# Kernel optimization log

Measured on AMD Instinct MI355X. Metric: run time of the kernel, lower is better.

Reference implementation:

```python
import jax, jax.numpy as jnp
import numpy as np

SELF_DIM = 64
NB_DIM = 64
HID = 256
K = 16  # num_use_neighbor_obs


def _ff(x, w1, b1, w2, b2):
    # FeedForward: Linear -> GELU (exact erf, torch nn.GELU default) -> Linear
    return jax.nn.gelu(x @ w1 + b1, approximate=False) @ w2 + b2


def setup_inputs() -> dict:
    key = jax.random.key(0)
    ks = jax.random.split(key, 9)
    B = 8192
    s = 0.02
    return {
        "self_obs": jax.random.normal(ks[0], (B, SELF_DIM), jnp.float32),
        "obs": jax.random.normal(ks[1], (B, SELF_DIM + K * NB_DIM), jnp.float32),
        "We1": jax.random.normal(ks[2], (SELF_DIM + NB_DIM, 4 * (SELF_DIM + NB_DIM)), jnp.float32) * s,
        "be1": jnp.zeros((4 * (SELF_DIM + NB_DIM),), jnp.float32),
        "We2": jax.random.normal(ks[3], (4 * (SELF_DIM + NB_DIM), HID), jnp.float32) * s,
        "be2": jnp.zeros((HID,), jnp.float32),
        "Wv1": jax.random.normal(ks[4], (HID, 4 * HID), jnp.float32) * s,
        "bv1": jnp.zeros((4 * HID,), jnp.float32),
        "Wv2": jax.random.normal(ks[5], (4 * HID, HID), jnp.float32) * s,
        "bv2": jnp.zeros((HID,), jnp.float32),
        "Wa1": jax.random.normal(ks[6], (2 * HID, 8 * HID), jnp.float32) * s,
        "ba1": jnp.zeros((8 * HID,), jnp.float32),
        "Wa2": jax.random.normal(ks[7], (8 * HID, 1), jnp.float32) * s,
        "ba2": jnp.zeros((1,), jnp.float32),
        "all_neighbor_obs_size": K * NB_DIM,
        "batch_size": 8192,
    }


def reference(self_obs, obs, We1, be1, We2, be2, Wv1, bv1, Wv2, bv2,
              Wa1, ba1, Wa2, ba2, all_neighbor_obs_size, batch_size):
    # neighbor obs: (B, K*nd) -> (B*K, nd), batch-major row order
    obs_neighbors = obs[:, SELF_DIM:SELF_DIM + all_neighbor_obs_size].reshape(-1, NB_DIM)
    # torch .repeat(K, 1): tiles the whole batch K times -> neighbor-major order
    self_obs_repeat = jnp.tile(self_obs, (K, 1))  # (K*B, self_dim)
    mlp_input = jnp.concatenate([self_obs_repeat, obs_neighbors], axis=1)
    neighbor_embeddings = _ff(mlp_input, We1, be1, We2, be2)          # (B*K, H)
    neighbor_values = _ff(neighbor_embeddings, Wv1, bv1, Wv2, bv2)    # (B*K, H)
    emb_mean = neighbor_embeddings.reshape(batch_size, -1, HID).mean(axis=1)  # (B, H)
    emb_mean_repeat = jnp.tile(emb_mean, (K, 1))                      # (K*B, H)
    attn_in = jnp.concatenate([neighbor_embeddings, emb_mean_repeat], axis=1)
    attn_logits = _ff(attn_in, Wa1, ba1, Wa2, ba2).reshape(batch_size, -1)  # (B, K)
    attn = jax.nn.softmax(attn_logits, axis=1).reshape(-1, 1)         # (B*K, 1)
    final = (attn * neighbor_values).reshape(batch_size, -1, HID).sum(axis=1)
    return final
```

## Files before the change

### kernel.cpp

```cpp
#include <hip/hip_runtime.h>
#include <hip/hip_bf16.h>

#define B_SZ 8192
#define KNB 16
#define BK 131072
#define ED 256

typedef __attribute__((ext_vector_type(8))) short short8v;
typedef __attribute__((ext_vector_type(4))) float floatx4;

static __device__ __forceinline__ unsigned short f2bf(float f) {
  unsigned int u = __float_as_uint(f);
  u = (u + 0x7FFFu + ((u >> 16) & 1u)) >> 16;
  return (unsigned short)u;
}
static __device__ __forceinline__ float bf2f(unsigned short u) {
  return __uint_as_float(((unsigned int)u) << 16);
}
static __device__ __forceinline__ float gelu_erf(float x) {
  return 0.5f * x * (1.0f + erff(x * 0.70710678118654752f));
}
static __device__ __forceinline__ float gelu_poly(float x) {
  float t = x * x;
  float p = fmaf(t, fmaf(t, fmaf(t, fmaf(t, 2.8935185185e-4f, -2.9761904762e-3f),
                                 2.5e-2f), -1.6666666667e-1f), 1.0f);
  return 0.5f * x * fmaf(0.79788456080286536f * x, p, 1.0f);
}

#define MFMA(a, b, c) __builtin_amdgcn_mfma_f32_16x16x32_bf16((a), (b), (c), 0, 0, 0)

static __device__ __forceinline__ void gll16(const void* g, void* l) {
  __builtin_amdgcn_global_load_lds(
      (const __attribute__((address_space(1))) unsigned int*)g,
      (__attribute__((address_space(3))) unsigned int*)l, 16, 0, 0);
}

__global__ void wt_kernel(const float* __restrict__ W, unsigned short* __restrict__ WT,
                          int K, int N) {
  int idx = blockIdx.x * 256 + threadIdx.x;
  if (idx >= K * N) return;
  int n = idx / K, k = idx - n * K;
  WT[idx] = f2bf(W[(size_t)k * N + n]);
}

__global__ __launch_bounds__(256) void k1_kernel(
    const float* __restrict__ self_obs, const float* __restrict__ obs,
    const unsigned short* __restrict__ We1T, const float* __restrict__ be1,
    const unsigned short* __restrict__ We2T, const float* __restrict__ be2,
    unsigned short* __restrict__ E, unsigned short* __restrict__ M) {
  __shared__ unsigned short Xt[64][136];
  __shared__ unsigned short Ht[64][136];
  const int tid = threadIdx.x;
  const int wave = tid >> 6, lane = tid & 63, g = lane >> 4, r = lane & 15;
  const int row0 = blockIdx.x * 64;

#pragma unroll
  for (int p = 0; p < 8; ++p) {
    int e4 = (p * 256 + tid) * 4;
    int i = e4 >> 7, c = e4 & 127;
    int gi = row0 + i;
    const float* src;
    if (c < 64) src = self_obs + (size_t)(gi & (B_SZ - 1)) * 64 + c;
    else        src = obs + (size_t)(gi >> 4) * 1088 + 64 + (gi & 15) * 64 + (c - 64);
    float4 v = *(const float4*)src;
    ushort4 w;
    w.x = f2bf(v.x); w.y = f2bf(v.y); w.z = f2bf(v.z); w.w = f2bf(v.w);
    *(ushort4*)&Xt[i][c] = w;
  }
  __syncthreads();

  floatx4 eacc[4][4];
#pragma unroll
  for (int a = 0; a < 4; ++a)
#pragma unroll
    for (int c2 = 0; c2 < 4; ++c2) eacc[a][c2] = (floatx4)0.0f;

  for (int chunk = 0; chunk < 4; ++chunk) {
    const int hbase = chunk * 128;
    floatx4 hacc[2][4];
#pragma unroll
    for (int a = 0; a < 2; ++a)
#pragma unroll
      for (int c2 = 0; c2 < 4; ++c2) hacc[a][c2] = (floatx4)0.0f;

#pragma unroll
    for (int kk = 0; kk < 4; ++kk) {
      short8v afr[4];
#pragma unroll
      for (int rt = 0; rt < 4; ++rt)
        afr[rt] = *(const short8v*)&Xt[rt * 16 + r][kk * 32 + g * 8];
#pragma unroll
      for (int ctl = 0; ctl < 2; ++ctl) {
        int col = hbase + wave * 32 + ctl * 16 + r;
        short8v bfr = *(const short8v*)&We1T[(size_t)col * 128 + kk * 32 + g * 8];
#pragma unroll
        for (int rt = 0; rt < 4; ++rt) hacc[ctl][rt] = MFMA(afr[rt], bfr, hacc[ctl][rt]);
      }
    }
#pragma unroll
    for (int ctl = 0; ctl < 2; ++ctl) {
      int col = hbase + wave * 32 + ctl * 16 + r;
      float bias = be1[col];
#pragma unroll
      for (int rt = 0; rt < 4; ++rt)
#pragma unroll
        for (int q = 0; q < 4; ++q) {
          float h = gelu_erf(hacc[ctl][rt][q] + bias);
          Ht[rt * 16 + g * 4 + q][wave * 32 + ctl * 16 + r] = f2bf(h);
        }
    }
    __syncthreads();
#pragma unroll
    for (int kk = 0; kk < 4; ++kk) {
      short8v afr[4];
#pragma unroll
      for (int rt = 0; rt < 4; ++rt)
        afr[rt] = *(const short8v*)&Ht[rt * 16 + r][kk * 32 + g * 8];
#pragma unroll
      for (int ct = 0; ct < 4; ++ct) {
        int col = wave * 64 + ct * 16 + r;
        short8v bfr = *(const short8v*)&We2T[(size_t)col * 512 + hbase + kk * 32 + g * 8];
#pragma unroll
        for (int rt = 0; rt < 4; ++rt) eacc[rt][ct] = MFMA(afr[rt], bfr, eacc[rt][ct]);
      }
    }
    __syncthreads();
  }

#pragma unroll
  for (int ct = 0; ct < 4; ++ct) {
    int col = wave * 64 + ct * 16 + r;
    float bias = be2[col];
#pragma unroll
    for (int rt = 0; rt < 4; ++rt) {
      float msum = 0.f;
#pragma unroll
      for (int q = 0; q < 4; ++q) {
        float e = eacc[rt][ct][q] + bias;
        int row = rt * 16 + g * 4 + q;
        E[(size_t)(row0 + row) * ED + col] = f2bf(e);
        msum += e;
      }
      msum += __shfl_xor(msum, 16);
      msum += __shfl_xor(msum, 32);
      if (g == 0) {
        int b = (row0 >> 4) + rt;
        M[(size_t)b * ED + col] = f2bf(msum * 0.0625f);
      }
    }
  }
}

__global__ __launch_bounds__(512) void k2_mv(
    const unsigned short* __restrict__ M, const unsigned short* __restrict__ Wa1T,
    const float* __restrict__ ba1, unsigned short* __restrict__ MV) {
  __shared__ unsigned short Abuf[128 * 64];
  __shared__ unsigned short Bbuf[256 * 64];
  const int tid = threadIdx.x;
  const int wave = tid >> 6, lane = tid & 63, g = lane >> 4, r = lane & 15;
  const int wr = wave >> 2, wc = wave & 3;
  const int row0 = blockIdx.y * 128;
  const int col0 = blockIdx.x * 256;
  const int sr = lane >> 3, sc = lane & 7;
  const int swz = ((sc ^ sr) << 4);

  floatx4 acc[4][4];
#pragma unroll
  for (int a = 0; a < 4; ++a)
#pragma unroll
    for (int c2 = 0; c2 < 4; ++c2) acc[a][c2] = (floatx4)0.0f;

  for (int t = 0; t < 4; ++t) {
#pragma unroll
    for (int j = 0; j < 2; ++j) {
      int rowA = j * 64 + wave * 8 + sr;
      const char* src = (const char*)M + ((size_t)(row0 + rowA)) * 512 + t * 128 + swz;
      gll16(src, (char*)Abuf + (j * 512 + wave * 64) * 16);
    }
#pragma unroll
    for (int j = 0; j < 4; ++j) {
      int colB = j * 64 + wave * 8 + sr;
      const char* src = (const char*)Wa1T + ((size_t)(col0 + colB)) * 1024 + 512
                        + t * 128 + swz;
      gll16(src, (char*)Bbuf + (j * 512 + wave * 64) * 16);
    }
    __syncthreads();
#pragma unroll
    for (int kk = 0; kk < 2; ++kk) {
      const int off = (kk * 64 + g * 16) ^ ((r & 7) << 4);
      short8v afr[4], bfr[4];
#pragma unroll
      for (int rt = 0; rt < 4; ++rt)
        afr[rt] = *(const short8v*)((const char*)Abuf + (wr * 64 + rt * 16 + r) * 128 + off);
#pragma unroll
      for (int ct = 0; ct < 4; ++ct)
        bfr[ct] = *(const short8v*)((const char*)Bbuf + (wc * 64 + ct * 16 + r) * 128 + off);
#pragma unroll
      for (int rt = 0; rt < 4; ++rt)
#pragma unroll
        for (int ct = 0; ct < 4; ++ct) acc[rt][ct] = MFMA(afr[rt], bfr[ct], acc[rt][ct]);
    }
    __syncthreads();
  }

#pragma unroll
  for (int ct = 0; ct < 4; ++ct) {
    int col = col0 + wc * 64 + ct * 16 + r;
    float b1 = ba1[col];
#pragma unroll
    for (int rt = 0; rt < 4; ++rt)
#pragma unroll
      for (int q = 0; q < 4; ++q)
        MV[(size_t)(row0 + wr * 64 + rt * 16 + g * 4 + q) * 2048 + col] =
            f2bf(acc[rt][ct][q] + b1);
  }
}

__global__ __launch_bounds__(512, 4) void k3_fused(
    const unsigned short* __restrict__ E, const unsigned short* __restrict__ MV,
    const unsigned short* __restrict__ Wa1T, const float* __restrict__ Wa2,
    float* __restrict__ L) {
  __shared__ char Bq[65536];
  const int tid = threadIdx.x;
  const int wave = tid >> 6, lane = tid & 63, g = lane >> 4, r = lane & 15;
  const int j = blockIdx.x * 8 + wave;
  const int xsw = (r & 7) << 4;

  const unsigned short* ebase = E + ((size_t)r * 8192 + j) * 256 + g * 8;
  short8v er[8];
#pragma unroll
  for (int kk = 0; kk < 8; ++kk) er[kk] = *(const short8v*)(ebase + kk * 32);

  const int scol2 = lane >> 5;
  const int sbyte = (lane & 31) * 16;

  auto STAGE = [&](int c, int bufsel) {
#pragma unroll
    for (int cc = 0; cc < 4; ++cc) {
      int m = wave * 4 + cc;
      int col = c * 64 + m * 2 + scol2;
      const char* src = (const char*)Wa1T + (size_t)col * 1024
                        + (sbyte ^ ((col & 7) << 4));
      gll16(src, Bq + bufsel * 32768 + m * 1024);
    }
  };

  STAGE(0, 0);
  __syncthreads();

  float lg = 0.f;
  const unsigned short* mvrow = MV + (size_t)j * 2048;

  for (int c = 0; c < 32; ++c) {
    if (c + 1 < 32) STAGE(c + 1, (c + 1) & 1);
    ushort4 mvu[4];
    float4 w2[4];
#pragma unroll
    for (int ct = 0; ct < 4; ++ct) {
      mvu[ct] = *(const ushort4*)(mvrow + c * 64 + ct * 16 + g * 4);
      w2[ct] = *(const float4*)&Wa2[c * 64 + ct * 16 + g * 4];
    }
    floatx4 acc[4];
#pragma unroll
    for (int ct = 0; ct < 4; ++ct) acc[ct] = (floatx4)0.0f;
    const char* bufb = Bq + (c & 1) * 32768;
#pragma unroll
    for (int kk = 0; kk < 8; ++kk) {
      const int off = (kk * 64 + g * 16) ^ xsw;
#pragma unroll
      for (int ct = 0; ct < 4; ++ct) {
        short8v a = *(const short8v*)(bufb + (ct * 16 + r) * 512 + off);
        acc[ct] = MFMA(a, er[kk], acc[ct]);
      }
    }
#pragma unroll
    for (int ct = 0; ct < 4; ++ct) {
      const float* wp = (const float*)&w2[ct];
      lg = fmaf(gelu_poly(acc[ct][0] + bf2f(mvu[ct].x)), wp[0], lg);
      lg = fmaf(gelu_poly(acc[ct][1] + bf2f(mvu[ct].y)), wp[1], lg);
      lg = fmaf(gelu_poly(acc[ct][2] + bf2f(mvu[ct].z)), wp[2], lg);
      lg = fmaf(gelu_poly(acc[ct][3] + bf2f(mvu[ct].w)), wp[3], lg);
    }
    __syncthreads();
  }

  lg += __shfl_xor(lg, 16);
  lg += __shfl_xor(lg, 32);
  if (g == 0) L[(size_t)r * 8192 + j] = lg;
}

__global__ __launch_bounds__(256) void k4_softmax(
    const float* __restrict__ L, const float* __restrict__ ba2,
    float* __restrict__ attnw) {
  int row = blockIdx.x * 256 + threadIdx.x;
  float logit = L[row] + ba2[0];
  float m = logit;
  m = fmaxf(m, __shfl_xor(m, 1)); m = fmaxf(m, __shfl_xor(m, 2));
  m = fmaxf(m, __shfl_xor(m, 4)); m = fmaxf(m, __shfl_xor(m, 8));
  float e = expf(logit - m);
  float s = e;
  s += __shfl_xor(s, 1); s += __shfl_xor(s, 2);
  s += __shfl_xor(s, 4); s += __shfl_xor(s, 8);
  attnw[row] = e / s;
}

__global__ __launch_bounds__(512) void k5a_gemm(
    const unsigned short* __restrict__ E, const unsigned short* __restrict__ Wv1T,
    const float* __restrict__ bv1, const float* __restrict__ attnw,
    unsigned short* __restrict__ G) {
  __shared__ unsigned short Abuf[128 * 64];
  __shared__ unsigned short Bbuf[256 * 64];
  const int tid = threadIdx.x;
  const int wave = tid >> 6, lane = tid & 63, g = lane >> 4, r = lane & 15;
  const int wr = wave >> 2, wc = wave & 3;
  const int nb = blockIdx.x;
  const int row0 = blockIdx.y * 128;
  const int col0 = nb * 256;
  const int sr = lane >> 3, sc = lane & 7;
  const int swz = ((sc ^ sr) << 4);

  floatx4 acc[4][4];
#pragma unroll
  for (int a = 0; a < 4; ++a)
#pragma unroll
    for (int c2 = 0; c2 < 4; ++c2) acc[a][c2] = (floatx4)0.0f;

  for (int t = 0; t < 4; ++t) {
#pragma unroll
    for (int j = 0; j < 2; ++j) {
      int rowA = j * 64 + wave * 8 + sr;
      const char* src = (const char*)E + ((size_t)(row0 + rowA)) * 512 + t * 128 + swz;
      gll16(src, (char*)Abuf + (j * 512 + wave * 64) * 16);
    }
#pragma unroll
    for (int j = 0; j < 4; ++j) {
      int colB = j * 64 + wave * 8 + sr;
      const char* src = (const char*)Wv1T + ((size_t)(col0 + colB)) * 512 + t * 128 + swz;
      gll16(src, (char*)Bbuf + (j * 512 + wave * 64) * 16);
    }
    __syncthreads();
#pragma unroll
    for (int kk = 0; kk < 2; ++kk) {
      const int off = (kk * 64 + g * 16) ^ ((r & 7) << 4);
      short8v afr[4], bfr[4];
#pragma unroll
      for (int rt = 0; rt < 4; ++rt)
        afr[rt] = *(const short8v*)((const char*)Abuf + (wr * 64 + rt * 16 + r) * 128 + off);
#pragma unroll
      for (int ct = 0; ct < 4; ++ct)
        bfr[ct] = *(const short8v*)((const char*)Bbuf + (wc * 64 + ct * 16 + r) * 128 + off);
#pragma unroll
      for (int rt = 0; rt < 4; ++rt)
#pragma unroll
        for (int ct = 0; ct < 4; ++ct) acc[rt][ct] = MFMA(afr[rt], bfr[ct], acc[rt][ct]);
    }
    __syncthreads();
  }

  float aw[4][4];
#pragma unroll
  for (int rt = 0; rt < 4; ++rt)
#pragma unroll
    for (int q = 0; q < 4; ++q)
      aw[rt][q] = attnw[row0 + wr * 64 + rt * 16 + g * 4 + q];
#pragma unroll
  for (int ct = 0; ct < 4; ++ct) {
    int col = col0 + wc * 64 + ct * 16 + r;
    float b1 = bv1[col];
#pragma unroll
    for (int rt = 0; rt < 4; ++rt) {
      float s = 0.f;
#pragma unroll
      for (int q = 0; q < 4; ++q)
        s = fmaf(aw[rt][q], gelu_poly(acc[rt][ct][q] + b1), s);
      s += __shfl_xor(s, 16);
      s += __shfl_xor(s, 32);
      if (g == 0)
        G[(size_t)((row0 >> 4) + wr * 4 + rt) * 1024 + col] = f2bf(s);
    }
  }
}

__global__ __launch_bounds__(256) void k5b_gemm(
    const unsigned short* __restrict__ G, const unsigned short* __restrict__ Wv2T,
    const float* __restrict__ bv2, float* __restrict__ out) {
  __shared__ unsigned short Abuf[64 * 64];
  __shared__ unsigned short Bbuf[128 * 64];
  const int tid = threadIdx.x;
  const int wave = tid >> 6, lane = tid & 63, g = lane >> 4, r = lane & 15;
  const int wr = wave >> 1, wc = wave & 1;
  const int col0 = blockIdx.x * 128;
  const int row0 = blockIdx.y * 64;
  const int sr = lane >> 3, sc = lane & 7;
  const int swz = ((sc ^ sr) << 4);

  floatx4 acc[2][4];
#pragma unroll
  for (int a = 0; a < 2; ++a)
#pragma unroll
    for (int c2 = 0; c2 < 4; ++c2) acc[a][c2] = (floatx4)0.0f;

  for (int t = 0; t < 16; ++t) {
#pragma unroll
    for (int j = 0; j < 2; ++j) {
      int rowA = j * 32 + wave * 8 + sr;
      const char* src = (const char*)G + ((size_t)(row0 + rowA)) * 2048 + t * 128 + swz;
      gll16(src, (char*)Abuf + (j * 256 + wave * 64) * 16);
    }
#pragma unroll
    for (int j = 0; j < 4; ++j) {
      int colB = j * 32 + wave * 8 + sr;
      const char* src = (const char*)Wv2T + ((size_t)(col0 + colB)) * 2048 + t * 128 + swz;
      gll16(src, (char*)Bbuf + (j * 256 + wave * 64) * 16);
    }
    __syncthreads();
#pragma unroll
    for (int kk = 0; kk < 2; ++kk) {
      const int off = (kk * 64 + g * 16) ^ ((r & 7) << 4);
      short8v afr[2], bfr[4];
#pragma unroll
      for (int rt = 0; rt < 2; ++rt)
        afr[rt] = *(const short8v*)((const char*)Abuf + (wr * 32 + rt * 16 + r) * 128 + off);
#pragma unroll
      for (int ct = 0; ct < 4; ++ct)
        bfr[ct] = *(const short8v*)((const char*)Bbuf + (wc * 64 + ct * 16 + r) * 128 + off);
#pragma unroll
      for (int rt = 0; rt < 2; ++rt)
#pragma unroll
        for (int ct = 0; ct < 4; ++ct) acc[rt][ct] = MFMA(afr[rt], bfr[ct], acc[rt][ct]);
    }
    __syncthreads();
  }

#pragma unroll
  for (int ct = 0; ct < 4; ++ct) {
    int col = col0 + wc * 64 + ct * 16 + r;
    float b = bv2[col];
#pragma unroll
    for (int rt = 0; rt < 2; ++rt)
#pragma unroll
      for (int q = 0; q < 4; ++q)
        out[(size_t)(row0 + wr * 32 + rt * 16 + g * 4 + q) * ED + col] =
            acc[rt][ct][q] + b;
  }
}

extern "C" void kernel_launch(void* const* d_in, const int* in_sizes, int n_in,
                              void* d_out, int out_size, void* d_ws, size_t ws_size,
                              hipStream_t stream) {
  const float* self_obs = (const float*)d_in[0];
  const float* obs = (const float*)d_in[1];
  const float* We1 = (const float*)d_in[2];
  const float* be1 = (const float*)d_in[3];
  const float* We2 = (const float*)d_in[4];
  const float* be2 = (const float*)d_in[5];
  const float* Wv1 = (const float*)d_in[6];
  const float* bv1 = (const float*)d_in[7];
  const float* Wv2 = (const float*)d_in[8];
  const float* bv2 = (const float*)d_in[9];
  const float* Wa1 = (const float*)d_in[10];
  const float* ba1 = (const float*)d_in[11];
  const float* Wa2 = (const float*)d_in[12];
  const float* ba2 = (const float*)d_in[13];
  float* out = (float*)d_out;

  char* ws = (char*)d_ws;
  size_t off = 0;
  auto alloc = [&](size_t bytes) {
    char* p = ws + off;
    off += (bytes + 255) & ~(size_t)255;
    return p;
  };
  unsigned short* E    = (unsigned short*)alloc((size_t)BK * ED * 2);
  unsigned short* M    = (unsigned short*)alloc((size_t)B_SZ * ED * 2);
  float*          attn = (float*)alloc((size_t)BK * 4);
  unsigned short* MV   = (unsigned short*)alloc((size_t)B_SZ * 2048 * 2);
  float*          L    = (float*)alloc((size_t)BK * 4);
  unsigned short* We1T = (unsigned short*)alloc(128 * 512 * 2);
  unsigned short* We2T = (unsigned short*)alloc(512 * 256 * 2);
  unsigned short* Wv1T = (unsigned short*)alloc(256 * 1024 * 2);
  unsigned short* Wv2T = (unsigned short*)alloc(1024 * 256 * 2);
  unsigned short* Wa1T = (unsigned short*)alloc(512 * 2048 * 2);
  unsigned short* G    = (unsigned short*)MV;

  wt_kernel<<<(128 * 512 + 255) / 256, 256, 0, stream>>>(We1, We1T, 128, 512);
  wt_kernel<<<(512 * 256 + 255) / 256, 256, 0, stream>>>(We2, We2T, 512, 256);
  wt_kernel<<<(256 * 1024 + 255) / 256, 256, 0, stream>>>(Wv1, Wv1T, 256, 1024);
  wt_kernel<<<(1024 * 256 + 255) / 256, 256, 0, stream>>>(Wv2, Wv2T, 1024, 256);
  wt_kernel<<<(512 * 2048 + 255) / 256, 256, 0, stream>>>(Wa1, Wa1T, 512, 2048);

  k1_kernel<<<BK / 64, 256, 0, stream>>>(self_obs, obs, We1T, be1, We2T, be2, E, M);
  k2_mv<<<dim3(8, 64), 512, 0, stream>>>(M, Wa1T, ba1, MV);
  k3_fused<<<B_SZ / 8, 512, 0, stream>>>(E, MV, Wa1T, Wa2, L);
  k4_softmax<<<BK / 256, 256, 0, stream>>>(L, ba2, attn);
  k5a_gemm<<<dim3(4, 1024), 512, 0, stream>>>(E, Wv1T, bv1, attn, G);
  k5b_gemm<<<dim3(2, 128), 256, 0, stream>>>(G, Wv2T, bv2, out);
}
```

Baseline: 504.2 us.

## Pre-swizzle Wa1 into MFMA fragment layout and process two batch rows per wave

A new prep kernel writes the first half of Wa1 (its first 256 input rows) into bf16 laid out in MFMA A-fragment order, so LDS staging and fragment reads become contiguous per-lane 16-byte accesses with no XOR swizzle. In k3 each wave now handles two batch columns, reusing every LDS-loaded weight fragment for two MFMAs. The column chunk shrinks from 64 to 32, which halves LDS use but doubles the number of loop iterations and barriers. Register pressure rises from holding two E fragment sets and two accumulator sets per wave, and the grid is halved.

```diff
diff --git a/kernel.cpp b/kernel.cpp
--- a/kernel.cpp
+++ b/kernel.cpp
@@ -41,6 +41,18 @@
   if (idx >= K * N) return;
   int n = idx / K, k = idx - n * K;
   WT[idx] = f2bf(W[(size_t)k * N + n]);
+}
+
+__global__ void wa1f_kernel(const float* __restrict__ Wa1,
+                            unsigned short* __restrict__ Wa1F) {
+  int idx = blockIdx.x * 256 + threadIdx.x;
+  int f = idx >> 9;
+  int w = idx & 511;
+  int ln = w >> 3, i = w & 7;
+  int ctile = f >> 3, kk = f & 7;
+  int col = ctile * 16 + (ln & 15);
+  int k = kk * 32 + (ln >> 4) * 8 + i;
+  Wa1F[idx] = f2bf(Wa1[(size_t)k * 2048 + col]);
 }
 
 __global__ __launch_bounds__(256) void k1_kernel(
@@ -218,75 +230,83 @@
 
 __global__ __launch_bounds__(512, 4) void k3_fused(
     const unsigned short* __restrict__ E, const unsigned short* __restrict__ MV,
-    const unsigned short* __restrict__ Wa1T, const float* __restrict__ Wa2,
+    const unsigned short* __restrict__ Wa1F, const float* __restrict__ Wa2,
     float* __restrict__ L) {
-  __shared__ char Bq[65536];
+  __shared__ char Bq[32768];
   const int tid = threadIdx.x;
   const int wave = tid >> 6, lane = tid & 63, g = lane >> 4, r = lane & 15;
-  const int j = blockIdx.x * 8 + wave;
-  const int xsw = (r & 7) << 4;
-
-  const unsigned short* ebase = E + ((size_t)r * 8192 + j) * 256 + g * 8;
-  short8v er[8];
-#pragma unroll
-  for (int kk = 0; kk < 8; ++kk) er[kk] = *(const short8v*)(ebase + kk * 32);
-
-  const int scol2 = lane >> 5;
-  const int sbyte = (lane & 31) * 16;
+  const int j0 = blockIdx.x * 16 + wave * 2;
+
+  short8v er0[8], er1[8];
+  {
+    const unsigned short* e0 = E + ((size_t)r * 8192 + j0) * 256 + g * 8;
+    const unsigned short* e1 = e0 + 256;
+#pragma unroll
+    for (int kk = 0; kk < 8; ++kk) {
+      er0[kk] = *(const short8v*)(e0 + kk * 32);
+      er1[kk] = *(const short8v*)(e1 + kk * 32);
+    }
+  }
 
   auto STAGE = [&](int c, int bufsel) {
 #pragma unroll
-    for (int cc = 0; cc < 4; ++cc) {
-      int m = wave * 4 + cc;
-      int col = c * 64 + m * 2 + scol2;
-      const char* src = (const char*)Wa1T + (size_t)col * 1024
-                        + (sbyte ^ ((col & 7) << 4));
-      gll16(src, Bq + bufsel * 32768 + m * 1024);
+    for (int cc = 0; cc < 2; ++cc) {
+      const char* src = (const char*)Wa1F + (size_t)c * 16384
+                        + (wave * 2 + cc) * 1024 + lane * 16;
+      gll16(src, Bq + bufsel * 16384 + (wave * 2 + cc) * 1024);
     }
   };
 
   STAGE(0, 0);
   __syncthreads();
 
-  float lg = 0.f;
-  const unsigned short* mvrow = MV + (size_t)j * 2048;
-
-  for (int c = 0; c < 32; ++c) {
-    if (c + 1 < 32) STAGE(c + 1, (c + 1) & 1);
-    ushort4 mvu[4];
-    float4 w2[4];
-#pragma unroll
-    for (int ct = 0; ct < 4; ++ct) {
-      mvu[ct] = *(const ushort4*)(mvrow + c * 64 + ct * 16 + g * 4);
-      w2[ct] = *(const float4*)&Wa2[c * 64 + ct * 16 + g * 4];
-    }
-    floatx4 acc[4];
-#pragma unroll
-    for (int ct = 0; ct < 4; ++ct) acc[ct] = (floatx4)0.0f;
-    const char* bufb = Bq + (c & 1) * 32768;
+  float lgp0 = 0.f, lgp1 = 0.f;
+  const unsigned short* mv0 = MV + (size_t)j0 * 2048;
+  const unsigned short* mv1 = mv0 + 2048;
+
+  for (int c = 0; c < 64; ++c) {
+    if (c + 1 < 64) STAGE(c + 1, (c + 1) & 1);
+    ushort4 mq0[2], mq1[2];
+    float4 w2[2];
+#pragma unroll
+    for (int ct = 0; ct < 2; ++ct) {
+      mq0[ct] = *(const ushort4*)(mv0 + c * 32 + ct * 16 + g * 4);
+      mq1[ct] = *(const ushort4*)(mv1 + c * 32 + ct * 16 + g * 4);
+      w2[ct] = *(const float4*)&Wa2[c * 32 + ct * 16 + g * 4];
+    }
+    floatx4 acc0[2], acc1[2];
+    acc0[0] = (floatx4)0.0f; acc0[1] = (floatx4)0.0f;
+    acc1[0] = (floatx4)0.0f; acc1[1] = (floatx4)0.0f;
+    const char* bufb = Bq + (c & 1) * 16384;
 #pragma unroll
     for (int kk = 0; kk < 8; ++kk) {
-      const int off = (kk * 64 + g * 16) ^ xsw;
-#pragma unroll
-      for (int ct = 0; ct < 4; ++ct) {
-        short8v a = *(const short8v*)(bufb + (ct * 16 + r) * 512 + off);
-        acc[ct] = MFMA(a, er[kk], acc[ct]);
+#pragma unroll
+      for (int ct = 0; ct < 2; ++ct) {
+        short8v a = *(const short8v*)(bufb + (ct * 8 + kk) * 1024 + lane * 16);
+        acc0[ct] = MFMA(a, er0[kk], acc0[ct]);
+        acc1[ct] = MFMA(a, er1[kk], acc1[ct]);
       }
     }
 #pragma unroll
-    for (int ct = 0; ct < 4; ++ct) {
+    for (int ct = 0; ct < 2; ++ct) {
       const float* wp = (const float*)&w2[ct];
-      lg = fmaf(gelu_poly(acc[ct][0] + bf2f(mvu[ct].x)), wp[0], lg);
-      lg = fmaf(gelu_poly(acc[ct][1] + bf2f(mvu[ct].y)), wp[1], lg);
-      lg = fmaf(gelu_poly(acc[ct][2] + bf2f(mvu[ct].z)), wp[2], lg);
-      lg = fmaf(gelu_poly(acc[ct][3] + bf2f(mvu[ct].w)), wp[3], lg);
-    }
-    __syncthreads();
-  }
-
-  lg += __shfl_xor(lg, 16);
-  lg += __shfl_xor(lg, 32);
-  if (g == 0) L[(size_t)r * 8192 + j] = lg;
+      const unsigned short* m0p = (const unsigned short*)&mq0[ct];
+      const unsigned short* m1p = (const unsigned short*)&mq1[ct];
+#pragma unroll
+      for (int q = 0; q < 4; ++q) {
+        lgp0 = fmaf(gelu_poly(acc0[ct][q] + bf2f(m0p[q])), wp[q], lgp0);
+        lgp1 = fmaf(gelu_poly(acc1[ct][q] + bf2f(m1p[q])), wp[q], lgp1);
+      }
+    }
+    __syncthreads();
+  }
+
+  lgp0 += __shfl_xor(lgp0, 16); lgp0 += __shfl_xor(lgp0, 32);
+  lgp1 += __shfl_xor(lgp1, 16); lgp1 += __shfl_xor(lgp1, 32);
+  if (g == 0) {
+    L[(size_t)r * 8192 + j0] = lgp0;
+    L[(size_t)r * 8192 + j0 + 1] = lgp1;
+  }
 }
 
 __global__ __launch_bounds__(256) void k4_softmax(
@@ -481,6 +501,7 @@
   unsigned short* Wv1T = (unsigned short*)alloc(256 * 1024 * 2);
   unsigned short* Wv2T = (unsigned short*)alloc(1024 * 256 * 2);
   unsigned short* Wa1T = (unsigned short*)alloc(512 * 2048 * 2);
+  unsigned short* Wa1F = (unsigned short*)alloc(2048 * 256 * 2);
   unsigned short* G    = (unsigned short*)MV;
 
   wt_kernel<<<(128 * 512 + 255) / 256, 256, 0, stream>>>(We1, We1T, 128, 512);
@@ -488,10 +509,11 @@
   wt_kernel<<<(256 * 1024 + 255) / 256, 256, 0, stream>>>(Wv1, Wv1T, 256, 1024);
   wt_kernel<<<(1024 * 256 + 255) / 256, 256, 0, stream>>>(Wv2, Wv2T, 1024, 256);
   wt_kernel<<<(512 * 2048 + 255) / 256, 256, 0, stream>>>(Wa1, Wa1T, 512, 2048);
+  wa1f_kernel<<<2048, 256, 0, stream>>>(Wa1, Wa1F);
 
   k1_kernel<<<BK / 64, 256, 0, stream>>>(self_obs, obs, We1T, be1, We2T, be2, E, M);
   k2_mv<<<dim3(8, 64), 512, 0, stream>>>(M, Wa1T, ba1, MV);
-  k3_fused<<<B_SZ / 8, 512, 0, stream>>>(E, MV, Wa1T, Wa2, L);
+  k3_fused<<<B_SZ / 16, 512, 0, stream>>>(E, MV, Wa1F, Wa2, L);
   k4_softmax<<<BK / 256, 256, 0, stream>>>(L, ba2, attn);
   k5a_gemm<<<dim3(4, 1024), 512, 0, stream>>>(E, Wv1T, bv1, attn, G);
   k5b_gemm<<<dim3(2, 128), 256, 0, stream>>>(G, Wv2T, bv2, out);
```

Measured after the change: 484.2 us. -4.0%, faster.
